# Kernel tuning notes

Hardware: AMD Instinct MI355X
Metric: run time of the kernel (lower is better)

Reference implementation:

```python
import jax, jax.numpy as jnp
import numpy as np

RADIUS = [1.0, 1.5, 2.0, 100.0]  # bucket boundaries; last is catch-all
NFILT = len(RADIUS)
C_IN, C_OUT = 256, 512


def setup_inputs() -> dict:
    key = jax.random.key(0)
    k1, k2, k3, k4 = jax.random.split(key, 4)
    b, n = 16, 4096
    feat = jax.random.normal(k1, (b, n, C_IN), dtype=jnp.float32)
    xyz = jax.random.normal(k2, (b, n, 3), dtype=jnp.float32)
    # init per original reset_parameters
    std = 2.0 * np.sqrt(2.0 / (C_IN + C_OUT))
    a = np.sqrt(3.0) * std
    weight = jax.random.uniform(k3, (NFILT, C_OUT, C_IN), dtype=jnp.float32, minval=-a, maxval=a)
    bound = 1.0 / np.sqrt(C_IN)
    bias = jax.random.uniform(k4, (NFILT, C_OUT), dtype=jnp.float32, minval=-bound, maxval=bound)
    return {"feat": feat, "xyz": xyz, "weight": weight, "bias": bias}


def reference(feat, xyz, weight, bias):
    b, n, c = feat.shape
    p = feat.reshape(b * n, c)                      # (P, C)
    radii = jnp.asarray(RADIUS, dtype=feat.dtype)
    r_norm = jnp.linalg.norm(xyz.reshape(b * n, 3), axis=1)
    # first radius with r_norm < r (same as the sequential break in map2filtId)
    filt_id = jnp.argmax(r_norm[:, None] < radii[None, :], axis=1)  # (P,)
    # grouped linear expressed densely: all Nfilt GEMMs, then per-point select
    all_out = jnp.einsum('pc,foc->fpo', p, weight) + bias[:, None, :]  # (F, P, O)
    out = jnp.take_along_axis(all_out, filt_id[None, :, None], axis=0)[0]  # (P, O)
    return out.reshape(b, n, -1)
```

## Files before the change

kernel.cpp:

```cpp
#include <hip/hip_runtime.h>
#include <hip/hip_bf16.h>

#define C_IN   256
#define C_OUT  512
#define NFILT  4

#define BM 128
#define BN 128
#define BK 32
#define SAS 40

typedef __attribute__((ext_vector_type(8))) short bf16x8;
typedef __attribute__((ext_vector_type(4))) float floatx4;

union Pack8 { uint4 u; __hip_bfloat16 h[8]; };

__global__ void zero_cnt_kernel(int* __restrict__ cnt) {
    if (threadIdx.x < NFILT) cnt[threadIdx.x] = 0;
}

__global__ void bucketize_kernel(const float* __restrict__ xyz,
                                 int* __restrict__ idxbuf,
                                 int* __restrict__ cnt, int P) {
    int pid = blockIdx.x * blockDim.x + threadIdx.x;
    if (pid >= P) return;
    float x = xyz[pid * 3 + 0];
    float y = xyz[pid * 3 + 1];
    float z = xyz[pid * 3 + 2];
    float r2 = __fadd_rn(__fadd_rn(__fmul_rn(x, x), __fmul_rn(y, y)), __fmul_rn(z, z));
    float r = sqrtf(r2);
    int filt;
    if (r < 1.0f)        filt = 0;
    else if (r < 1.5f)   filt = 1;
    else if (r < 2.0f)   filt = 2;
    else if (r < 100.0f) filt = 3;
    else                 filt = 0;

    int lane = threadIdx.x & 63;
    for (int f = 0; f < NFILT; ++f) {
        unsigned long long mask = __ballot(filt == f);
        if (mask == 0ull) continue;
        int leader = __ffsll((unsigned long long)mask) - 1;
        int base = 0;
        if (lane == leader) base = atomicAdd(&cnt[f], __popcll(mask));
        base = __shfl(base, leader);
        if (filt == f) {
            int off = __popcll(mask & ((1ull << lane) - 1ull));
            idxbuf[f * P + base + off] = pid;
        }
    }
}

__global__ void convert_w_kernel(const float* __restrict__ w,
                                 ushort* __restrict__ wb) {
    int i = (blockIdx.x * blockDim.x + threadIdx.x) * 4;
    float4 v = *(const float4*)(w + i);
    union { ushort4 u; __hip_bfloat16 h[4]; } cv;
    cv.h[0] = __float2bfloat16(v.x);
    cv.h[1] = __float2bfloat16(v.y);
    cv.h[2] = __float2bfloat16(v.z);
    cv.h[3] = __float2bfloat16(v.w);
    *(ushort4*)(wb + i) = cv.u;
}

__global__ __launch_bounds__(256) void gemm_kernel(
    const float* __restrict__ feat, const ushort* __restrict__ wb,
    const float* __restrict__ bias, const int* __restrict__ idxbuf,
    const int* __restrict__ cnt, float* __restrict__ out, int P)
{
    __shared__ ushort sA[BM * SAS];
    __shared__ ushort sB[BN * SAS];
    __shared__ int    sIdx[BM];
    __shared__ float  sBias[BN];

    int t = blockIdx.y;
    int counts[4];
    counts[0] = cnt[0]; counts[1] = cnt[1]; counts[2] = cnt[2]; counts[3] = cnt[3];
    int f = -1, lt = 0;
    for (int ff = 0; ff < 4; ++ff) {
        int nt = (counts[ff] + BM - 1) / BM;
        if (t < nt) { f = ff; lt = t; break; }
        t -= nt;
    }
    if (f < 0) return;

    int tid = threadIdx.x;
    int oBase = blockIdx.x * BN;
    int rowBase = lt * BM;
    int cn = counts[f];

    if (tid < BM) {
        int r = rowBase + tid;
        sIdx[tid] = (r < cn) ? idxbuf[f * P + r] : -1;
    }
    if (tid < BN) sBias[tid] = bias[f * C_OUT + oBase + tid];
    __syncthreads();

    int sRow = tid >> 1;
    int sHalf = tid & 1;
    int myIdx = sIdx[sRow];
    const float* aRow = feat + (size_t)(myIdx < 0 ? 0 : myIdx) * C_IN + sHalf * 16;
    const ushort* bRow = wb + (size_t)(f * C_OUT + oBase + sRow) * C_IN + sHalf * 16;

    int wid = tid >> 6;
    int lane = tid & 63;
    int wm = (wid >> 1) * 64;
    int wn = (wid & 1) * 64;
    int lcol = lane & 15;
    int quad = lane >> 4;

    floatx4 acc[4][4];
#pragma unroll
    for (int i = 0; i < 4; ++i)
#pragma unroll
        for (int j = 0; j < 4; ++j)
            acc[i][j] = (floatx4){0.f, 0.f, 0.f, 0.f};

    for (int kk = 0; kk < C_IN; kk += BK) {
        const float* ap = aRow + kk;
        float4 a0 = *(const float4*)(ap + 0);
        float4 a1 = *(const float4*)(ap + 4);
        float4 a2 = *(const float4*)(ap + 8);
        float4 a3 = *(const float4*)(ap + 12);
        const ushort* bp = bRow + kk;
        uint4 b01 = *(const uint4*)(bp + 0);
        uint4 b23 = *(const uint4*)(bp + 8);

        Pack8 p0, p1;
        p0.h[0] = __float2bfloat16(a0.x); p0.h[1] = __float2bfloat16(a0.y);
        p0.h[2] = __float2bfloat16(a0.z); p0.h[3] = __float2bfloat16(a0.w);
        p0.h[4] = __float2bfloat16(a1.x); p0.h[5] = __float2bfloat16(a1.y);
        p0.h[6] = __float2bfloat16(a1.z); p0.h[7] = __float2bfloat16(a1.w);
        p1.h[0] = __float2bfloat16(a2.x); p1.h[1] = __float2bfloat16(a2.y);
        p1.h[2] = __float2bfloat16(a2.z); p1.h[3] = __float2bfloat16(a2.w);
        p1.h[4] = __float2bfloat16(a3.x); p1.h[5] = __float2bfloat16(a3.y);
        p1.h[6] = __float2bfloat16(a3.z); p1.h[7] = __float2bfloat16(a3.w);

        ushort* dA = &sA[sRow * SAS + sHalf * 16];
        *(uint4*)(dA + 0) = p0.u;
        *(uint4*)(dA + 8) = p1.u;
        ushort* dB = &sB[sRow * SAS + sHalf * 16];
        *(uint4*)(dB + 0) = b01;
        *(uint4*)(dB + 8) = b23;

        __syncthreads();

        bf16x8 af[4], bfr[4];
#pragma unroll
        for (int i = 0; i < 4; ++i)
            af[i] = *(const bf16x8*)&sA[(wm + i * 16 + lcol) * SAS + quad * 8];
#pragma unroll
        for (int j = 0; j < 4; ++j)
            bfr[j] = *(const bf16x8*)&sB[(wn + j * 16 + lcol) * SAS + quad * 8];
#pragma unroll
        for (int i = 0; i < 4; ++i)
#pragma unroll
            for (int j = 0; j < 4; ++j)
                acc[i][j] = __builtin_amdgcn_mfma_f32_16x16x32_bf16(af[i], bfr[j], acc[i][j], 0, 0, 0);

        __syncthreads();
    }

#pragma unroll
    for (int i = 0; i < 4; ++i) {
        int r0 = wm + i * 16 + quad * 4;
        int pid0 = sIdx[r0 + 0];
        int pid1 = sIdx[r0 + 1];
        int pid2 = sIdx[r0 + 2];
        int pid3 = sIdx[r0 + 3];
#pragma unroll
        for (int j = 0; j < 4; ++j) {
            int o = oBase + wn + j * 16 + lcol;
            float bv = sBias[wn + j * 16 + lcol];
            if (pid0 >= 0) out[pid0 * C_OUT + o] = acc[i][j][0] + bv;
            if (pid1 >= 0) out[pid1 * C_OUT + o] = acc[i][j][1] + bv;
            if (pid2 >= 0) out[pid2 * C_OUT + o] = acc[i][j][2] + bv;
            if (pid3 >= 0) out[pid3 * C_OUT + o] = acc[i][j][3] + bv;
        }
    }
}

extern "C" void kernel_launch(void* const* d_in, const int* in_sizes, int n_in,
                              void* d_out, int out_size, void* d_ws, size_t ws_size,
                              hipStream_t stream) {
    const float* feat = (const float*)d_in[0];
    const float* xyz  = (const float*)d_in[1];
    const float* w    = (const float*)d_in[2];
    const float* bias = (const float*)d_in[3];
    float* out = (float*)d_out;
    int P = in_sizes[0] / C_IN;

    char* ws = (char*)d_ws;
    int* idxbuf = (int*)ws;
    int* cntp   = (int*)(ws + (size_t)4 * P * 4);
    ushort* wb  = (ushort*)(ws + (size_t)4 * P * 4 + 16);

    zero_cnt_kernel<<<1, 64, 0, stream>>>(cntp);
    bucketize_kernel<<<(P + 255) / 256, 256, 0, stream>>>(xyz, idxbuf, cntp, P);
    convert_w_kernel<<<(NFILT * C_OUT * C_IN) / 1024, 256, 0, stream>>>(w, wb);

    dim3 grid(C_OUT / BN, P / BM + NFILT);
    gemm_kernel<<<grid, 256, 0, stream>>>(feat, wb, bias, idxbuf, cntp, out, P);
}
```

Baseline: 274.9 us.

## Prefetch next K-slice into registers, remap block order, fold counter zeroing into weight conversion

The GEMM main loop now loads the next K-slice of gathered features and weights into registers while the current slice is converted and run through MFMA, hiding global gather latency. The syncthreads calls become explicit waitcnt, barrier and sched_barrier. Block indices are remapped so groups of 8 row tiles run their 4 output-column tiles together, which should improve L2 reuse of the gathered feature rows. The separate counter-zeroing kernel is folded into the weight conversion kernel, removing one launch. The prefetch raises register pressure, and the grid is padded to a multiple of 8 rows; the extra blocks exit early.

```diff
diff --git a/kernel.cpp b/kernel.cpp
--- a/kernel.cpp
+++ b/kernel.cpp
@@ -14,10 +14,6 @@
 typedef __attribute__((ext_vector_type(4))) float floatx4;
 
 union Pack8 { uint4 u; __hip_bfloat16 h[8]; };
-
-__global__ void zero_cnt_kernel(int* __restrict__ cnt) {
-    if (threadIdx.x < NFILT) cnt[threadIdx.x] = 0;
-}
 
 __global__ void bucketize_kernel(const float* __restrict__ xyz,
                                  int* __restrict__ idxbuf,
@@ -52,7 +48,9 @@
 }
 
 __global__ void convert_w_kernel(const float* __restrict__ w,
-                                 ushort* __restrict__ wb) {
+                                 ushort* __restrict__ wb,
+                                 int* __restrict__ cnt) {
+    if (blockIdx.x == 0 && threadIdx.x < NFILT) cnt[threadIdx.x] = 0;
     int i = (blockIdx.x * blockDim.x + threadIdx.x) * 4;
     float4 v = *(const float4*)(w + i);
     union { ushort4 u; __hip_bfloat16 h[4]; } cv;
@@ -73,7 +71,12 @@
     __shared__ int    sIdx[BM];
     __shared__ float  sBias[BN];
 
-    int t = blockIdx.y;
+    int lid = blockIdx.x + (blockIdx.y << 2);
+    int g = lid & 7;
+    int q = lid >> 3;
+    int cTile = q & 3;
+    int t = ((q >> 2) << 3) + g;
+
     int counts[4];
     counts[0] = cnt[0]; counts[1] = cnt[1]; counts[2] = cnt[2]; counts[3] = cnt[3];
     int f = -1, lt = 0;
@@ -85,7 +88,7 @@
     if (f < 0) return;
 
     int tid = threadIdx.x;
-    int oBase = blockIdx.x * BN;
+    int oBase = cTile * BN;
     int rowBase = lt * BM;
     int cn = counts[f];
 
@@ -116,15 +119,30 @@
         for (int j = 0; j < 4; ++j)
             acc[i][j] = (floatx4){0.f, 0.f, 0.f, 0.f};
 
-    for (int kk = 0; kk < C_IN; kk += BK) {
-        const float* ap = aRow + kk;
-        float4 a0 = *(const float4*)(ap + 0);
-        float4 a1 = *(const float4*)(ap + 4);
-        float4 a2 = *(const float4*)(ap + 8);
-        float4 a3 = *(const float4*)(ap + 12);
-        const ushort* bp = bRow + kk;
-        uint4 b01 = *(const uint4*)(bp + 0);
-        uint4 b23 = *(const uint4*)(bp + 8);
+    ushort* dA = &sA[sRow * SAS + sHalf * 16];
+    ushort* dB = &sB[sRow * SAS + sHalf * 16];
+
+    float4 a0 = *(const float4*)(aRow + 0);
+    float4 a1 = *(const float4*)(aRow + 4);
+    float4 a2 = *(const float4*)(aRow + 8);
+    float4 a3 = *(const float4*)(aRow + 12);
+    uint4  b01 = *(const uint4*)(bRow + 0);
+    uint4  b23 = *(const uint4*)(bRow + 8);
+
+#pragma unroll
+    for (int s = 0; s < 8; ++s) {
+        float4 n0, n1, n2, n3;
+        uint4  nb01, nb23;
+        if (s < 7) {
+            const float*  ap = aRow + (s + 1) * BK;
+            const ushort* bp = bRow + (s + 1) * BK;
+            n0   = *(const float4*)(ap + 0);
+            n1   = *(const float4*)(ap + 4);
+            n2   = *(const float4*)(ap + 8);
+            n3   = *(const float4*)(ap + 12);
+            nb01 = *(const uint4*)(bp + 0);
+            nb23 = *(const uint4*)(bp + 8);
+        }
 
         Pack8 p0, p1;
         p0.h[0] = __float2bfloat16(a0.x); p0.h[1] = __float2bfloat16(a0.y);
@@ -135,15 +153,14 @@
         p1.h[2] = __float2bfloat16(a2.z); p1.h[3] = __float2bfloat16(a2.w);
         p1.h[4] = __float2bfloat16(a3.x); p1.h[5] = __float2bfloat16(a3.y);
         p1.h[6] = __float2bfloat16(a3.z); p1.h[7] = __float2bfloat16(a3.w);
-
-        ushort* dA = &sA[sRow * SAS + sHalf * 16];
         *(uint4*)(dA + 0) = p0.u;
         *(uint4*)(dA + 8) = p1.u;
-        ushort* dB = &sB[sRow * SAS + sHalf * 16];
         *(uint4*)(dB + 0) = b01;
         *(uint4*)(dB + 8) = b23;
 
-        __syncthreads();
+        asm volatile("s_waitcnt lgkmcnt(0)" ::: "memory");
+        __builtin_amdgcn_s_barrier();
+        __builtin_amdgcn_sched_barrier(0);
 
         bf16x8 af[4], bfr[4];
 #pragma unroll
@@ -158,7 +175,14 @@
             for (int j = 0; j < 4; ++j)
                 acc[i][j] = __builtin_amdgcn_mfma_f32_16x16x32_bf16(af[i], bfr[j], acc[i][j], 0, 0, 0);
 
-        __syncthreads();
+        asm volatile("s_waitcnt lgkmcnt(0)" ::: "memory");
+        __builtin_amdgcn_s_barrier();
+        __builtin_amdgcn_sched_barrier(0);
+
+        if (s < 7) {
+            a0 = n0; a1 = n1; a2 = n2; a3 = n3;
+            b01 = nb01; b23 = nb23;
+        }
     }
 
 #pragma unroll
@@ -195,10 +219,10 @@
     int* cntp   = (int*)(ws + (size_t)4 * P * 4);
     ushort* wb  = (ushort*)(ws + (size_t)4 * P * 4 + 16);
 
-    zero_cnt_kernel<<<1, 64, 0, stream>>>(cntp);
+    convert_w_kernel<<<(NFILT * C_OUT * C_IN) / 1024, 256, 0, stream>>>(w, wb, cntp);
     bucketize_kernel<<<(P + 255) / 256, 256, 0, stream>>>(xyz, idxbuf, cntp, P);
-    convert_w_kernel<<<(NFILT * C_OUT * C_IN) / 1024, 256, 0, stream>>>(w, wb);
-
-    dim3 grid(C_OUT / BN, P / BM + NFILT);
+
+    int tilesY = ((P / BM + NFILT + 7) / 8) * 8;
+    dim3 grid(C_OUT / BN, tilesY);
     gemm_kernel<<<grid, 256, 0, stream>>>(feat, wb, bias, idxbuf, cntp, out, P);
 }
```

Result: no change. 279.9 us (+1.8%).

## Pre-gather bf16 activations and stream tiles via direct global-to-LDS loads

Applied to the files above, without the earlier changes.

A new gather kernel compacts the rows into bucket-sorted bf16 order in workspace. A new GEMM kernel then loads contiguous A and B tiles straight into LDS with global_load_lds, using a 64-wide K step and an XOR swizzle. Tile indices are remapped so groups of 8 row tiles share a column tile for better cache reuse, and the counter zeroing is folded into the weight conversion kernel to save a launch. This adds an extra pass over the activations and workspace memory, and falls back to the old kernel if the workspace is too small.

```diff
diff --git a/kernel.cpp b/kernel.cpp
--- a/kernel.cpp
+++ b/kernel.cpp
@@ -10,14 +10,12 @@
 #define BK 32
 #define SAS 40
 
+#define FBK 64
+
 typedef __attribute__((ext_vector_type(8))) short bf16x8;
 typedef __attribute__((ext_vector_type(4))) float floatx4;
 
 union Pack8 { uint4 u; __hip_bfloat16 h[8]; };
-
-__global__ void zero_cnt_kernel(int* __restrict__ cnt) {
-    if (threadIdx.x < NFILT) cnt[threadIdx.x] = 0;
-}
 
 __global__ void bucketize_kernel(const float* __restrict__ xyz,
                                  int* __restrict__ idxbuf,
@@ -52,7 +50,9 @@
 }
 
 __global__ void convert_w_kernel(const float* __restrict__ w,
-                                 ushort* __restrict__ wb) {
+                                 ushort* __restrict__ wb,
+                                 int* __restrict__ cnt) {
+    if (blockIdx.x == 0 && threadIdx.x < NFILT) cnt[threadIdx.x] = 0;
     int i = (blockIdx.x * blockDim.x + threadIdx.x) * 4;
     float4 v = *(const float4*)(w + i);
     union { ushort4 u; __hip_bfloat16 h[4]; } cv;
@@ -61,6 +61,151 @@
     cv.h[2] = __float2bfloat16(v.z);
     cv.h[3] = __float2bfloat16(v.w);
     *(ushort4*)(wb + i) = cv.u;
+}
+
+__global__ __launch_bounds__(256) void gather_kernel(
+    const float* __restrict__ feat, const int* __restrict__ idxbuf,
+    const int* __restrict__ cnt, ushort* __restrict__ gA, int P)
+{
+    int wid = threadIdx.x >> 6;
+    int lane = threadIdx.x & 63;
+    int slot = blockIdx.x * 4 + wid;
+    if (slot >= P) return;
+    int c0 = cnt[0], c1 = cnt[1], c2 = cnt[2];
+    int b1 = c0, b2 = c0 + c1, b3 = c0 + c1 + c2;
+    int f, i;
+    if (slot < b1)      { f = 0; i = slot; }
+    else if (slot < b2) { f = 1; i = slot - b1; }
+    else if (slot < b3) { f = 2; i = slot - b2; }
+    else                { f = 3; i = slot - b3; }
+    int pid = idxbuf[f * P + i];
+    float4 v = *(const float4*)(feat + (size_t)pid * C_IN + lane * 4);
+    union { ushort4 u; __hip_bfloat16 h[4]; } cv;
+    cv.h[0] = __float2bfloat16(v.x);
+    cv.h[1] = __float2bfloat16(v.y);
+    cv.h[2] = __float2bfloat16(v.z);
+    cv.h[3] = __float2bfloat16(v.w);
+    *(ushort4*)(gA + (size_t)slot * C_IN + lane * 4) = cv.u;
+}
+
+__global__ __launch_bounds__(256) void gemm_fast_kernel(
+    const ushort* __restrict__ gA, const ushort* __restrict__ wb,
+    const float* __restrict__ bias, const int* __restrict__ idxbuf,
+    const int* __restrict__ cnt, float* __restrict__ out, int P)
+{
+    __shared__ ushort sA[BM * FBK];
+    __shared__ ushort sB[BN * FBK];
+    __shared__ int    sIdx[BM];
+    __shared__ float  sBias[BN];
+
+    int lid = blockIdx.x + (blockIdx.y << 2);
+    int g = lid & 7;
+    int q = lid >> 3;
+    int cTile = q & 3;
+    int t = ((q >> 2) << 3) + g;
+
+    int c0 = cnt[0], c1 = cnt[1], c2 = cnt[2], c3 = cnt[3];
+    int counts[4] = {c0, c1, c2, c3};
+    int bases[4]  = {0, c0, c0 + c1, c0 + c1 + c2};
+    int f = -1, lt = 0;
+    for (int ff = 0; ff < 4; ++ff) {
+        int nt = (counts[ff] + BM - 1) / BM;
+        if (t < nt) { f = ff; lt = t; break; }
+        t -= nt;
+    }
+    if (f < 0) return;
+
+    int tid = threadIdx.x;
+    int oBase = cTile * BN;
+    int cn = counts[f];
+    int gBase = bases[f] + lt * BM;
+    int wRow0 = f * C_OUT + oBase;
+
+    if (tid < BM) {
+        int r = lt * BM + tid;
+        sIdx[tid] = (r < cn) ? idxbuf[f * P + r] : -1;
+    }
+    if (tid < BN) sBias[tid] = bias[f * C_OUT + oBase + tid];
+    __syncthreads();
+
+    int wid = tid >> 6;
+    int lane = tid & 63;
+    int wm = (wid >> 1) * 64;
+    int wn = (wid & 1) * 64;
+    int lcol = lane & 15;
+    int quad = lane >> 4;
+    int rp = lcol & 7;
+
+    int lrow = lane >> 3;
+    int lchunk = lane & 7;
+    int schunk = lchunk ^ lrow;
+
+    floatx4 acc[4][4];
+#pragma unroll
+    for (int i = 0; i < 4; ++i)
+#pragma unroll
+        for (int j = 0; j < 4; ++j)
+            acc[i][j] = (floatx4){0.f, 0.f, 0.f, 0.f};
+
+    const char* aBase = (const char*)gA;
+    const char* bBase = (const char*)wb;
+
+#pragma unroll
+    for (int s = 0; s < C_IN / FBK; ++s) {
+        int kByte = s * (FBK * 2);
+#pragma unroll
+        for (int n = 0; n < 4; ++n) {
+            int seg = wid * 4 + n;
+            int row = seg * 8 + lrow;
+            const char* srcA = aBase + ((size_t)(gBase + row) * (C_IN * 2)) + kByte + schunk * 16;
+            __builtin_amdgcn_global_load_lds(
+                (const __attribute__((address_space(1))) void*)srcA,
+                (__attribute__((address_space(3))) void*)&sA[seg * 512], 16, 0, 0);
+            const char* srcB = bBase + ((size_t)(wRow0 + row) * (C_IN * 2)) + kByte + schunk * 16;
+            __builtin_amdgcn_global_load_lds(
+                (const __attribute__((address_space(1))) void*)srcB,
+                (__attribute__((address_space(3))) void*)&sB[seg * 512], 16, 0, 0);
+        }
+        asm volatile("s_waitcnt vmcnt(0)" ::: "memory");
+        __builtin_amdgcn_s_barrier();
+        __builtin_amdgcn_sched_barrier(0);
+
+#pragma unroll
+        for (int kk2 = 0; kk2 < 2; ++kk2) {
+            int ck = ((kk2 * 4 + quad) ^ rp) * 8;
+            bf16x8 af[4], bfr[4];
+#pragma unroll
+            for (int i = 0; i < 4; ++i)
+                af[i] = *(const bf16x8*)&sA[(wm + i * 16 + lcol) * FBK + ck];
+#pragma unroll
+            for (int j = 0; j < 4; ++j)
+                bfr[j] = *(const bf16x8*)&sB[(wn + j * 16 + lcol) * FBK + ck];
+#pragma unroll
+            for (int i = 0; i < 4; ++i)
+#pragma unroll
+                for (int j = 0; j < 4; ++j)
+                    acc[i][j] = __builtin_amdgcn_mfma_f32_16x16x32_bf16(af[i], bfr[j], acc[i][j], 0, 0, 0);
+        }
+        if (s < C_IN / FBK - 1) __syncthreads();
+    }
+
+#pragma unroll
+    for (int i = 0; i < 4; ++i) {
+        int r0 = wm + i * 16 + quad * 4;
+        int pid0 = sIdx[r0 + 0];
+        int pid1 = sIdx[r0 + 1];
+        int pid2 = sIdx[r0 + 2];
+        int pid3 = sIdx[r0 + 3];
+#pragma unroll
+        for (int j = 0; j < 4; ++j) {
+            int o = oBase + wn + j * 16 + lcol;
+            float bv = sBias[wn + j * 16 + lcol];
+            if (pid0 >= 0) out[pid0 * C_OUT + o] = acc[i][j][0] + bv;
+            if (pid1 >= 0) out[pid1 * C_OUT + o] = acc[i][j][1] + bv;
+            if (pid2 >= 0) out[pid2 * C_OUT + o] = acc[i][j][2] + bv;
+            if (pid3 >= 0) out[pid3 * C_OUT + o] = acc[i][j][3] + bv;
+        }
+    }
 }
 
 __global__ __launch_bounds__(256) void gemm_kernel(
@@ -73,7 +218,12 @@
     __shared__ int    sIdx[BM];
     __shared__ float  sBias[BN];
 
-    int t = blockIdx.y;
+    int lid = blockIdx.x + (blockIdx.y << 2);
+    int g = lid & 7;
+    int q = lid >> 3;
+    int cTile = q & 3;
+    int t = ((q >> 2) << 3) + g;
+
     int counts[4];
     counts[0] = cnt[0]; counts[1] = cnt[1]; counts[2] = cnt[2]; counts[3] = cnt[3];
     int f = -1, lt = 0;
@@ -85,7 +235,7 @@
     if (f < 0) return;
 
     int tid = threadIdx.x;
-    int oBase = blockIdx.x * BN;
+    int oBase = cTile * BN;
     int rowBase = lt * BM;
     int cn = counts[f];
 
@@ -191,14 +341,27 @@
     int P = in_sizes[0] / C_IN;
 
     char* ws = (char*)d_ws;
-    int* idxbuf = (int*)ws;
-    int* cntp   = (int*)(ws + (size_t)4 * P * 4);
-    ushort* wb  = (ushort*)(ws + (size_t)4 * P * 4 + 16);
-
-    zero_cnt_kernel<<<1, 64, 0, stream>>>(cntp);
+    size_t offIdx = 0;
+    size_t offCnt = (size_t)4 * P * 4;
+    size_t offWb  = offCnt + 16;
+    size_t offGA  = (offWb + (size_t)NFILT * C_OUT * C_IN * 2 + 255) & ~(size_t)255;
+    size_t needed = offGA + (size_t)(P + BM) * C_IN * 2;
+
+    int* idxbuf = (int*)(ws + offIdx);
+    int* cntp   = (int*)(ws + offCnt);
+    ushort* wb  = (ushort*)(ws + offWb);
+
+    convert_w_kernel<<<(NFILT * C_OUT * C_IN) / 1024, 256, 0, stream>>>(w, wb, cntp);
     bucketize_kernel<<<(P + 255) / 256, 256, 0, stream>>>(xyz, idxbuf, cntp, P);
-    convert_w_kernel<<<(NFILT * C_OUT * C_IN) / 1024, 256, 0, stream>>>(w, wb);
-
-    dim3 grid(C_OUT / BN, P / BM + NFILT);
-    gemm_kernel<<<grid, 256, 0, stream>>>(feat, wb, bias, idxbuf, cntp, out, P);
-}
+
+    int tilesY = ((P / BM + NFILT + 7) / 8) * 8;
+    dim3 grid(C_OUT / BN, tilesY);
+
+    if (ws_size >= needed) {
+        ushort* gA = (ushort*)(ws + offGA);
+        gather_kernel<<<(P + 3) / 4, 256, 0, stream>>>(feat, idxbuf, cntp, gA, P);
+        gemm_fast_kernel<<<grid, 256, 0, stream>>>(gA, wb, bias, idxbuf, cntp, out, P);
+    } else {
+        gemm_kernel<<<grid, 256, 0, stream>>>(feat, wb, bias, idxbuf, cntp, out, P);
+    }
+}
```

After: 278.4 us. No clear change (+1.3%).
